# Kernel optimization log

Measured on AMD Instinct MI355X. Metric: run time of the kernel, lower is better.

Reference implementation:

```python
import jax, jax.numpy as jnp
import numpy as np

N_NODES = 100000
N_EDGES = 600000
VOCAB = 50000
EMBED_DIM = 128
HIDDEN_DIM = 128


def gcn_conv(h, W, b, src, dst, n_nodes):
    """PyG GCNConv: x' = D^{-1/2} (A+I) D^{-1/2} X W + b.
    src/dst already include self-loops."""
    hw = h @ W                                   # [N, out]
    deg = jnp.zeros((n_nodes,), hw.dtype).at[dst].add(1.0)   # in-degree incl. self-loop
    dinv = jax.lax.rsqrt(deg)                    # deg >= 1 thanks to self-loops
    norm = dinv[src] * dinv[dst]                 # [E+N]
    msgs = norm[:, None] * hw[src]               # gather [E+N, out]
    out = jnp.zeros_like(hw).at[dst].add(msgs)   # scatter-aggregate
    return out + b


def setup_inputs() -> dict:
    key = jax.random.key(0)
    ks = jax.random.split(key, 8)
    x = jax.random.randint(ks[0], (N_NODES,), 0, VOCAB, dtype=jnp.int64 if jax.config.jax_enable_x64 else jnp.int32)
    edge_index = jax.random.randint(ks[1], (2, N_EDGES), 0, N_NODES, dtype=jnp.int32)
    emb = jax.random.normal(ks[2], (VOCAB, EMBED_DIM), dtype=jnp.float32)
    # Glorot-style scale for GCN weights
    W1 = jax.random.normal(ks[3], (EMBED_DIM, HIDDEN_DIM), dtype=jnp.float32) * (1.0 / np.sqrt(EMBED_DIM))
    b1 = jnp.zeros((HIDDEN_DIM,), dtype=jnp.float32)
    W2 = jax.random.normal(ks[4], (HIDDEN_DIM, HIDDEN_DIM), dtype=jnp.float32) * (1.0 / np.sqrt(HIDDEN_DIM))
    b2 = jnp.zeros((HIDDEN_DIM,), dtype=jnp.float32)
    return {"x": x, "edge_index": edge_index, "emb": emb, "W1": W1, "b1": b1, "W2": W2, "b2": b2}


def reference(x, edge_index, emb, W1, b1, W2, b2):
    n = x.shape[0]
    loops = jnp.arange(n, dtype=edge_index.dtype)
    src = jnp.concatenate([edge_index[0], loops])  # add self-loops once
    dst = jnp.concatenate([edge_index[1], loops])
    h = emb[x]                                     # [N, embed_dim] embedding lookup
    h = jax.nn.relu(gcn_conv(h, W1, b1, src, dst, n))
    h = jax.nn.relu(gcn_conv(h, W2, b2, src, dst, n))
    return h
```

## Files before the change

### kernel.cpp

```cpp
#include <hip/hip_runtime.h>


#define NDIM 128
#define PAD_K 136
#define SCAN_IPT 4
#define SCAN_BLK 256
#define SCAN_IPB (SCAN_BLK * SCAN_IPT)

typedef __bf16 bf16x8 __attribute__((ext_vector_type(8)));
typedef __bf16 bf16x4 __attribute__((ext_vector_type(4)));
typedef float f32x4 __attribute__((ext_vector_type(4)));

__device__ __forceinline__ float bf2f(unsigned short u) {
    union { unsigned int i; float f; } c;
    c.i = (unsigned int)u << 16;
    return c.f;
}
__device__ __forceinline__ unsigned short f2bf(float f) {
    __bf16 b = (__bf16)f;
    return __builtin_bit_cast(unsigned short, b);
}

__global__ void degree_count(const int* __restrict__ dst, int* __restrict__ cnt, int E) {
    int e = blockIdx.x * blockDim.x + threadIdx.x;
    if (e < E) atomicAdd(&cnt[dst[e]], 1);
}

__global__ void scan_blocks(const int* __restrict__ in, int* __restrict__ out,
                            int* __restrict__ bsums, int n) {
    __shared__ int lds[SCAN_BLK];
    const int t = threadIdx.x;
    const int base = blockIdx.x * SCAN_IPB + t * SCAN_IPT;
    int v[SCAN_IPT];
    int s = 0;
#pragma unroll
    for (int k = 0; k < SCAN_IPT; ++k) { v[k] = (base + k < n) ? in[base + k] : 0; s += v[k]; }
    lds[t] = s;
    __syncthreads();
    for (int off = 1; off < SCAN_BLK; off <<= 1) {
        int x = (t >= off) ? lds[t - off] : 0;
        __syncthreads();
        lds[t] += x;
        __syncthreads();
    }
    if (t == SCAN_BLK - 1) bsums[blockIdx.x] = lds[t];
    int run = (t == 0) ? 0 : lds[t - 1];
#pragma unroll
    for (int k = 0; k < SCAN_IPT; ++k) {
        if (base + k < n) out[base + k] = run;
        run += v[k];
    }
}

__global__ void scan_partials(int* __restrict__ bsums, int nb) {
    __shared__ int lds[128];
    const int t = threadIdx.x;
    lds[t] = (t < nb) ? bsums[t] : 0;
    __syncthreads();
    for (int off = 1; off < 128; off <<= 1) {
        int x = (t >= off) ? lds[t - off] : 0;
        __syncthreads();
        lds[t] += x;
        __syncthreads();
    }
    if (t < nb) bsums[t] = (t == 0) ? 0 : lds[t - 1];
}

__global__ void add_offsets_dinv(int* __restrict__ rp, const int* __restrict__ bsums,
                                 const int* __restrict__ cnt, float* __restrict__ dinv,
                                 int n, int E) {
    int i = blockIdx.x * blockDim.x + threadIdx.x;
    if (i < n) {
        rp[i] += bsums[i / SCAN_IPB];
        dinv[i] = rsqrtf((float)cnt[i] + 1.0f);
    }
    if (i == 0) rp[n] = E;
}

__global__ void fill_edges(const int* __restrict__ src, const int* __restrict__ dst,
                           const int* __restrict__ rp, int* __restrict__ cur,
                           int* __restrict__ esrc, int E) {
    int e = blockIdx.x * blockDim.x + threadIdx.x;
    if (e >= E) return;
    int d = dst[e];
    int p = rp[d] + atomicAdd(&cur[d], 1);
    esrc[p] = src[e];
}

__global__ void wt_convert2(const float* __restrict__ W1, const float* __restrict__ W2,
                            unsigned short* __restrict__ WT1, unsigned short* __restrict__ WT2) {
    int c = blockIdx.x * blockDim.x + threadIdx.x;
    int cc = c & 16383;
    int j = cc >> 7, k = cc & 127;
    if (c < 16384) WT1[cc] = f2bf(W1[k * 128 + j]);
    else           WT2[cc] = f2bf(W2[k * 128 + j]);
}

template <int MODE, bool SCALE>
__global__ __launch_bounds__(256, 3)
void gemm_mfma(const void* __restrict__ Asrc, const unsigned short* __restrict__ WTb,
               const float* __restrict__ dinv, unsigned short* __restrict__ outb, int n) {
    __shared__ __bf16 sA[64 * PAD_K];
    __shared__ __bf16 sBT[128 * PAD_K];
    const int tid = threadIdx.x;
    const int rbase = blockIdx.x * 64;

    if (MODE == 0) {
        const float* A = (const float*)Asrc;
#pragma unroll
        for (int i = 0; i < 8; ++i) {
            int c = tid + i * 256;
            int r = c >> 5, c4 = c & 31;
            int gr = rbase + r;
            int srow = (gr < n) ? gr : (n - 1);
            float4 v = ((const float4*)A)[(size_t)srow * 32 + c4];
            bf16x4 w = { (__bf16)v.x, (__bf16)v.y, (__bf16)v.z, (__bf16)v.w };
            *(bf16x4*)&sA[r * PAD_K + c4 * 4] = w;
        }
    } else {
        const unsigned short* A = (const unsigned short*)Asrc;
#pragma unroll
        for (int i = 0; i < 4; ++i) {
            int c = tid + i * 256;
            int r = c >> 4, u = c & 15;
            int gr = rbase + r;
            int srow = (gr < n) ? gr : (n - 1);
            uint4 v = ((const uint4*)(A + (size_t)srow * 128))[u];
            *(uint4*)&sA[r * PAD_K + u * 8] = v;
        }
    }
    {
        const uint4* bsrc = (const uint4*)WTb;
#pragma unroll
        for (int i = 0; i < 8; ++i) {
            int c = tid + i * 256;
            int j = c >> 4, u = c & 15;
            *(uint4*)&sBT[j * PAD_K + u * 8] = bsrc[c];
        }
    }
    __syncthreads();

    const int wave = tid >> 6, lane = tid & 63;
    const int quad = lane >> 4, lrow = lane & 15;

    f32x4 acc[8];
#pragma unroll
    for (int nt = 0; nt < 8; ++nt) acc[nt] = (f32x4)0.0f;

#pragma unroll
    for (int ks = 0; ks < 4; ++ks) {
        const int kb = ks * 32 + quad * 8;
        bf16x8 a = *(const bf16x8*)&sA[(wave * 16 + lrow) * PAD_K + kb];
#pragma unroll
        for (int nt = 0; nt < 8; ++nt) {
            bf16x8 b = *(const bf16x8*)&sBT[(nt * 16 + lrow) * PAD_K + kb];
            acc[nt] = __builtin_amdgcn_mfma_f32_16x16x32_bf16(a, b, acc[nt], 0, 0, 0);
        }
    }

#pragma unroll
    for (int r = 0; r < 4; ++r) {
        int grow = rbase + wave * 16 + quad * 4 + r;
        if (grow < n) {
            float dsc = SCALE ? dinv[grow] : 1.0f;
            unsigned short* orow = outb + (size_t)grow * NDIM + lrow;
#pragma unroll
            for (int nt = 0; nt < 8; ++nt)
                orow[nt * 16] = f2bf(SCALE ? dsc * acc[nt][r] : acc[nt][r]);
        }
    }
}

__global__ void gather_scale(const unsigned short* __restrict__ tab, const int* __restrict__ x,
                             const float* __restrict__ dinv, unsigned short* __restrict__ vs,
                             int n) {
    int t = blockIdx.x * blockDim.x + threadIdx.x;
    int i = t >> 4, u = t & 15;
    if (i >= n) return;
    int row = x[i];
    float di = dinv[i];
    union { uint4 q; unsigned short s[8]; } a;
    a.q = ((const uint4*)(tab + (size_t)row * 128))[u];
#pragma unroll
    for (int k = 0; k < 8; ++k) a.s[k] = f2bf(di * bf2f(a.s[k]));
    ((uint4*)(vs + (size_t)i * 128))[u] = a.q;
}

template <bool OUT_BF16>
__global__ void aggregate_csr(const unsigned short* __restrict__ vs, const int* __restrict__ rp,
                              const int* __restrict__ esrc, const float* __restrict__ dinv,
                              const float* __restrict__ bias, void* __restrict__ out, int n) {
    int t = blockIdx.x * blockDim.x + threadIdx.x;
    int i = t >> 5, lane = t & 31;
    if (i >= n) return;
    const ushort4* vs4 = (const ushort4*)vs;
    ushort4 u = vs4[(size_t)i * 32 + lane];
    float4 acc = make_float4(bf2f(u.x), bf2f(u.y), bf2f(u.z), bf2f(u.w));
    int j = rp[i];
    const int end = rp[i + 1];
    for (; j + 4 <= end; j += 4) {
        int s0 = esrc[j], s1 = esrc[j + 1], s2 = esrc[j + 2], s3 = esrc[j + 3];
        ushort4 v0 = vs4[(size_t)s0 * 32 + lane];
        ushort4 v1 = vs4[(size_t)s1 * 32 + lane];
        ushort4 v2 = vs4[(size_t)s2 * 32 + lane];
        ushort4 v3 = vs4[(size_t)s3 * 32 + lane];
        acc.x += (bf2f(v0.x) + bf2f(v1.x)) + (bf2f(v2.x) + bf2f(v3.x));
        acc.y += (bf2f(v0.y) + bf2f(v1.y)) + (bf2f(v2.y) + bf2f(v3.y));
        acc.z += (bf2f(v0.z) + bf2f(v1.z)) + (bf2f(v2.z) + bf2f(v3.z));
        acc.w += (bf2f(v0.w) + bf2f(v1.w)) + (bf2f(v2.w) + bf2f(v3.w));
    }
    for (; j < end; ++j) {
        int s = esrc[j];
        ushort4 v = vs4[(size_t)s * 32 + lane];
        acc.x += bf2f(v.x);
        acc.y += bf2f(v.y);
        acc.z += bf2f(v.z);
        acc.w += bf2f(v.w);
    }
    float di = dinv[i];
    float4 b = ((const float4*)bias)[lane];
    acc.x = fmaxf(fmaf(di, acc.x, b.x), 0.0f);
    acc.y = fmaxf(fmaf(di, acc.y, b.y), 0.0f);
    acc.z = fmaxf(fmaf(di, acc.z, b.z), 0.0f);
    acc.w = fmaxf(fmaf(di, acc.w, b.w), 0.0f);
    if (OUT_BF16) {
        ushort4 o = make_ushort4(f2bf(acc.x), f2bf(acc.y), f2bf(acc.z), f2bf(acc.w));
        ((ushort4*)out)[(size_t)i * 32 + lane] = o;
    } else {
        ((float4*)out)[(size_t)i * 32 + lane] = acc;
    }
}

extern "C" void kernel_launch(void* const* d_in, const int* in_sizes, int n_in,
                              void* d_out, int out_size, void* d_ws, size_t ws_size,
                              hipStream_t stream) {
    const int* x = (const int*)d_in[0];
    const int* edge_index = (const int*)d_in[1];
    const float* emb = (const float*)d_in[2];
    const float* W1 = (const float*)d_in[3];
    const float* b1 = (const float*)d_in[4];
    const float* W2 = (const float*)d_in[5];
    const float* b2 = (const float*)d_in[6];
    float* out = (float*)d_out;

    const int N = in_sizes[0];
    const int E = in_sizes[1] / 2;
    const int V = in_sizes[2] / NDIM;
    const int* src = edge_index;
    const int* dst = edge_index + E;

    char* p = (char*)d_ws;
    auto alloc = [&](size_t bytes) {
        char* q = p;
        p += (bytes + 511) & ~(size_t)511;
        return q;
    };
    int* cnt = (int*)alloc((size_t)2 * N * sizeof(int));
    int* cur = cnt + N;
    int* rp = (int*)alloc((size_t)(N + 1) * sizeof(int));
    float* dinv = (float*)alloc((size_t)N * sizeof(float));
    int* bsums = (int*)alloc(128 * sizeof(int));
    int* esrc = (int*)alloc((size_t)E * sizeof(int));
    unsigned short* WT1 = (unsigned short*)alloc(16384 * sizeof(unsigned short));
    unsigned short* WT2 = (unsigned short*)alloc(16384 * sizeof(unsigned short));
    unsigned short* embW1 = (unsigned short*)alloc((size_t)V * NDIM * sizeof(unsigned short));
    unsigned short* vs1 = (unsigned short*)alloc((size_t)N * NDIM * sizeof(unsigned short));
    unsigned short* h1b = (unsigned short*)alloc((size_t)N * NDIM * sizeof(unsigned short));
    unsigned short* vs2 = (unsigned short*)alloc((size_t)N * NDIM * sizeof(unsigned short));
    (void)ws_size;

    const int NB = (N + SCAN_IPB - 1) / SCAN_IPB;

    hipMemsetAsync(cnt, 0, (size_t)2 * N * sizeof(int), stream);
    degree_count<<<(E + 255) / 256, 256, 0, stream>>>(dst, cnt, E);
    scan_blocks<<<NB, SCAN_BLK, 0, stream>>>(cnt, rp, bsums, N);
    scan_partials<<<1, 128, 0, stream>>>(bsums, NB);
    add_offsets_dinv<<<(N + 255) / 256, 256, 0, stream>>>(rp, bsums, cnt, dinv, N, E);
    fill_edges<<<(E + 255) / 256, 256, 0, stream>>>(src, dst, rp, cur, esrc, E);

    wt_convert2<<<128, 256, 0, stream>>>(W1, W2, WT1, WT2);

    const int agg_blocks = (int)(((size_t)N * 32 + 255) / 256);
    const int gs_blocks = (int)(((size_t)N * 16 + 255) / 256);

    gemm_mfma<0, false><<<(V + 63) / 64, 256, 0, stream>>>(emb, WT1, nullptr, embW1, V);
    gather_scale<<<gs_blocks, 256, 0, stream>>>(embW1, x, dinv, vs1, N);
    aggregate_csr<true><<<agg_blocks, 256, 0, stream>>>(vs1, rp, esrc, dinv, b1, h1b, N);
    gemm_mfma<1, true><<<(N + 63) / 64, 256, 0, stream>>>(h1b, WT2, dinv, vs2, N);
    aggregate_csr<false><<<agg_blocks, 256, 0, stream>>>(vs2, rp, esrc, dinv, b2, out, N);
}
```

Measured before the change: 258.4 us.

## Fuse embedding gather into layer-1 aggregation and streamline CSR build and GEMM loads

Removes the gather_scale kernel and its intermediate buffer. The first aggregation now reads the projected embedding table directly through a per-edge (vocab row, dinv) record written during CSR fill. The CSR fill uses atomicAdd on the row pointer itself, dropping the separate cursor array and the rp[n] write; row ranges become rp[i-1]..rp[i]. The GEMM drops the shared-memory A tile and loads A straight from global memory into registers, with launch bounds raised to 4 blocks per CU. Both aggregations now use 16 lanes per row with 16-byte loads. In exchange, fill_edges writes an extra 8 bytes per edge, and layer 1 gathers from the 50k-row table with per-edge scaling.

Measured after the change: 247.4 us. 4.2% less time.

```diff
diff --git a/kernel.cpp b/kernel.cpp
--- a/kernel.cpp
+++ b/kernel.cpp
@@ -8,7 +8,6 @@
 #define SCAN_IPB (SCAN_BLK * SCAN_IPT)
 
 typedef __bf16 bf16x8 __attribute__((ext_vector_type(8)));
-typedef __bf16 bf16x4 __attribute__((ext_vector_type(4)));
 typedef float f32x4 __attribute__((ext_vector_type(4)));
 
 __device__ __forceinline__ float bf2f(unsigned short u) {
@@ -19,6 +18,16 @@
 __device__ __forceinline__ unsigned short f2bf(float f) {
     __bf16 b = (__bf16)f;
     return __builtin_bit_cast(unsigned short, b);
+}
+__device__ __forceinline__ void unpack8(uint4 q, float* f) {
+    f[0] = bf2f((unsigned short)(q.x & 0xffff));
+    f[1] = bf2f((unsigned short)(q.x >> 16));
+    f[2] = bf2f((unsigned short)(q.y & 0xffff));
+    f[3] = bf2f((unsigned short)(q.y >> 16));
+    f[4] = bf2f((unsigned short)(q.z & 0xffff));
+    f[5] = bf2f((unsigned short)(q.z >> 16));
+    f[6] = bf2f((unsigned short)(q.w & 0xffff));
+    f[7] = bf2f((unsigned short)(q.w >> 16));
 }
 
 __global__ void degree_count(const int* __restrict__ dst, int* __restrict__ cnt, int E) {
@@ -67,24 +76,24 @@
 }
 
 __global__ void add_offsets_dinv(int* __restrict__ rp, const int* __restrict__ bsums,
-                                 const int* __restrict__ cnt, float* __restrict__ dinv,
-                                 int n, int E) {
+                                 const int* __restrict__ cnt, float* __restrict__ dinv, int n) {
     int i = blockIdx.x * blockDim.x + threadIdx.x;
     if (i < n) {
         rp[i] += bsums[i / SCAN_IPB];
         dinv[i] = rsqrtf((float)cnt[i] + 1.0f);
     }
-    if (i == 0) rp[n] = E;
 }
 
 __global__ void fill_edges(const int* __restrict__ src, const int* __restrict__ dst,
-                           const int* __restrict__ rp, int* __restrict__ cur,
-                           int* __restrict__ esrc, int E) {
+                           int* __restrict__ rp, const int* __restrict__ x,
+                           const float* __restrict__ dinv,
+                           int* __restrict__ esrc, int2* __restrict__ ew, int E) {
     int e = blockIdx.x * blockDim.x + threadIdx.x;
     if (e >= E) return;
-    int d = dst[e];
-    int p = rp[d] + atomicAdd(&cur[d], 1);
-    esrc[p] = src[e];
+    int d = dst[e], s = src[e];
+    int p = atomicAdd(&rp[d], 1);
+    esrc[p] = s;
+    ew[p] = make_int2(x[s], __float_as_int(dinv[s]));
 }
 
 __global__ void wt_convert2(const float* __restrict__ W1, const float* __restrict__ W2,
@@ -97,38 +106,13 @@
 }
 
 template <int MODE, bool SCALE>
-__global__ __launch_bounds__(256, 3)
+__global__ __launch_bounds__(256, 4)
 void gemm_mfma(const void* __restrict__ Asrc, const unsigned short* __restrict__ WTb,
                const float* __restrict__ dinv, unsigned short* __restrict__ outb, int n) {
-    __shared__ __bf16 sA[64 * PAD_K];
     __shared__ __bf16 sBT[128 * PAD_K];
     const int tid = threadIdx.x;
     const int rbase = blockIdx.x * 64;
 
-    if (MODE == 0) {
-        const float* A = (const float*)Asrc;
-#pragma unroll
-        for (int i = 0; i < 8; ++i) {
-            int c = tid + i * 256;
-            int r = c >> 5, c4 = c & 31;
-            int gr = rbase + r;
-            int srow = (gr < n) ? gr : (n - 1);
-            float4 v = ((const float4*)A)[(size_t)srow * 32 + c4];
-            bf16x4 w = { (__bf16)v.x, (__bf16)v.y, (__bf16)v.z, (__bf16)v.w };
-            *(bf16x4*)&sA[r * PAD_K + c4 * 4] = w;
-        }
-    } else {
-        const unsigned short* A = (const unsigned short*)Asrc;
-#pragma unroll
-        for (int i = 0; i < 4; ++i) {
-            int c = tid + i * 256;
-            int r = c >> 4, u = c & 15;
-            int gr = rbase + r;
-            int srow = (gr < n) ? gr : (n - 1);
-            uint4 v = ((const uint4*)(A + (size_t)srow * 128))[u];
-            *(uint4*)&sA[r * PAD_K + u * 8] = v;
-        }
-    }
     {
         const uint4* bsrc = (const uint4*)WTb;
 #pragma unroll
@@ -142,6 +126,8 @@
 
     const int wave = tid >> 6, lane = tid & 63;
     const int quad = lane >> 4, lrow = lane & 15;
+    int arow = rbase + wave * 16 + lrow;
+    if (arow >= n) arow = n - 1;
 
     f32x4 acc[8];
 #pragma unroll
@@ -150,7 +136,16 @@
 #pragma unroll
     for (int ks = 0; ks < 4; ++ks) {
         const int kb = ks * 32 + quad * 8;
-        bf16x8 a = *(const bf16x8*)&sA[(wave * 16 + lrow) * PAD_K + kb];
+        bf16x8 a;
+        if (MODE == 0) {
+            const float4* A4 = (const float4*)Asrc;
+            float4 v0 = A4[(size_t)arow * 32 + (kb >> 2)];
+            float4 v1 = A4[(size_t)arow * 32 + (kb >> 2) + 1];
+            a = (bf16x8){(__bf16)v0.x, (__bf16)v0.y, (__bf16)v0.z, (__bf16)v0.w,
+                         (__bf16)v1.x, (__bf16)v1.y, (__bf16)v1.z, (__bf16)v1.w};
+        } else {
+            a = *(const bf16x8*)((const unsigned short*)Asrc + (size_t)arow * 128 + kb);
+        }
 #pragma unroll
         for (int nt = 0; nt < 8; ++nt) {
             bf16x8 b = *(const bf16x8*)&sBT[(nt * 16 + lrow) * PAD_K + kb];
@@ -171,64 +166,113 @@
     }
 }
 
-__global__ void gather_scale(const unsigned short* __restrict__ tab, const int* __restrict__ x,
-                             const float* __restrict__ dinv, unsigned short* __restrict__ vs,
-                             int n) {
+__global__ void aggregate1(const unsigned short* __restrict__ tab, const int* __restrict__ x,
+                           const int* __restrict__ rp, const int2* __restrict__ ew,
+                           const float* __restrict__ dinv, const float* __restrict__ bias,
+                           unsigned short* __restrict__ outb, int n) {
     int t = blockIdx.x * blockDim.x + threadIdx.x;
     int i = t >> 4, u = t & 15;
     if (i >= n) return;
-    int row = x[i];
+    const uint4* tab4 = (const uint4*)tab;
     float di = dinv[i];
-    union { uint4 q; unsigned short s[8]; } a;
-    a.q = ((const uint4*)(tab + (size_t)row * 128))[u];
-#pragma unroll
-    for (int k = 0; k < 8; ++k) a.s[k] = f2bf(di * bf2f(a.s[k]));
-    ((uint4*)(vs + (size_t)i * 128))[u] = a.q;
-}
-
-template <bool OUT_BF16>
-__global__ void aggregate_csr(const unsigned short* __restrict__ vs, const int* __restrict__ rp,
-                              const int* __restrict__ esrc, const float* __restrict__ dinv,
-                              const float* __restrict__ bias, void* __restrict__ out, int n) {
+    float acc[8];
+    {
+        float f[8];
+        unpack8(tab4[(size_t)x[i] * 16 + u], f);
+#pragma unroll
+        for (int k = 0; k < 8; ++k) acc[k] = di * f[k];
+    }
+    int j = (i == 0) ? 0 : rp[i - 1];
+    const int end = rp[i];
+    for (; j + 4 <= end; j += 4) {
+        int2 e0 = ew[j], e1 = ew[j + 1], e2 = ew[j + 2], e3 = ew[j + 3];
+        uint4 q0 = tab4[(size_t)e0.x * 16 + u];
+        uint4 q1 = tab4[(size_t)e1.x * 16 + u];
+        uint4 q2 = tab4[(size_t)e2.x * 16 + u];
+        uint4 q3 = tab4[(size_t)e3.x * 16 + u];
+        float f0[8], f1[8], f2[8], f3[8];
+        unpack8(q0, f0); unpack8(q1, f1); unpack8(q2, f2); unpack8(q3, f3);
+        float n0 = __int_as_float(e0.y), n1 = __int_as_float(e1.y);
+        float n2 = __int_as_float(e2.y), n3 = __int_as_float(e3.y);
+#pragma unroll
+        for (int k = 0; k < 8; ++k) {
+            float s01 = fmaf(n0, f0[k], n1 * f1[k]);
+            float s23 = fmaf(n2, f2[k], n3 * f3[k]);
+            acc[k] += s01 + s23;
+        }
+    }
+    for (; j < end; ++j) {
+        int2 e = ew[j];
+        uint4 q = tab4[(size_t)e.x * 16 + u];
+        float f[8];
+        unpack8(q, f);
+        float nm = __int_as_float(e.y);
+#pragma unroll
+        for (int k = 0; k < 8; ++k) acc[k] = fmaf(nm, f[k], acc[k]);
+    }
+    const float4 b0 = ((const float4*)bias)[u * 2];
+    const float4 b1 = ((const float4*)bias)[u * 2 + 1];
+    float r[8];
+    r[0] = fmaxf(fmaf(di, acc[0], b0.x), 0.0f);
+    r[1] = fmaxf(fmaf(di, acc[1], b0.y), 0.0f);
+    r[2] = fmaxf(fmaf(di, acc[2], b0.z), 0.0f);
+    r[3] = fmaxf(fmaf(di, acc[3], b0.w), 0.0f);
+    r[4] = fmaxf(fmaf(di, acc[4], b1.x), 0.0f);
+    r[5] = fmaxf(fmaf(di, acc[5], b1.y), 0.0f);
+    r[6] = fmaxf(fmaf(di, acc[6], b1.z), 0.0f);
+    r[7] = fmaxf(fmaf(di, acc[7], b1.w), 0.0f);
+    uint4 o;
+    o.x = (unsigned)f2bf(r[0]) | ((unsigned)f2bf(r[1]) << 16);
+    o.y = (unsigned)f2bf(r[2]) | ((unsigned)f2bf(r[3]) << 16);
+    o.z = (unsigned)f2bf(r[4]) | ((unsigned)f2bf(r[5]) << 16);
+    o.w = (unsigned)f2bf(r[6]) | ((unsigned)f2bf(r[7]) << 16);
+    ((uint4*)outb)[(size_t)i * 16 + u] = o;
+}
+
+__global__ void aggregate2(const unsigned short* __restrict__ vs, const int* __restrict__ rp,
+                           const int* __restrict__ esrc, const float* __restrict__ dinv,
+                           const float* __restrict__ bias, float* __restrict__ out, int n) {
     int t = blockIdx.x * blockDim.x + threadIdx.x;
-    int i = t >> 5, lane = t & 31;
+    int i = t >> 4, u = t & 15;
     if (i >= n) return;
-    const ushort4* vs4 = (const ushort4*)vs;
-    ushort4 u = vs4[(size_t)i * 32 + lane];
-    float4 acc = make_float4(bf2f(u.x), bf2f(u.y), bf2f(u.z), bf2f(u.w));
-    int j = rp[i];
-    const int end = rp[i + 1];
+    const uint4* vs4 = (const uint4*)vs;
+    float acc[8];
+    unpack8(vs4[(size_t)i * 16 + u], acc);
+    int j = (i == 0) ? 0 : rp[i - 1];
+    const int end = rp[i];
     for (; j + 4 <= end; j += 4) {
         int s0 = esrc[j], s1 = esrc[j + 1], s2 = esrc[j + 2], s3 = esrc[j + 3];
-        ushort4 v0 = vs4[(size_t)s0 * 32 + lane];
-        ushort4 v1 = vs4[(size_t)s1 * 32 + lane];
-        ushort4 v2 = vs4[(size_t)s2 * 32 + lane];
-        ushort4 v3 = vs4[(size_t)s3 * 32 + lane];
-        acc.x += (bf2f(v0.x) + bf2f(v1.x)) + (bf2f(v2.x) + bf2f(v3.x));
-        acc.y += (bf2f(v0.y) + bf2f(v1.y)) + (bf2f(v2.y) + bf2f(v3.y));
-        acc.z += (bf2f(v0.z) + bf2f(v1.z)) + (bf2f(v2.z) + bf2f(v3.z));
-        acc.w += (bf2f(v0.w) + bf2f(v1.w)) + (bf2f(v2.w) + bf2f(v3.w));
+        uint4 q0 = vs4[(size_t)s0 * 16 + u];
+        uint4 q1 = vs4[(size_t)s1 * 16 + u];
+        uint4 q2 = vs4[(size_t)s2 * 16 + u];
+        uint4 q3 = vs4[(size_t)s3 * 16 + u];
+        float f0[8], f1[8], f2[8], f3[8];
+        unpack8(q0, f0); unpack8(q1, f1); unpack8(q2, f2); unpack8(q3, f3);
+#pragma unroll
+        for (int k = 0; k < 8; ++k) acc[k] += (f0[k] + f1[k]) + (f2[k] + f3[k]);
     }
     for (; j < end; ++j) {
         int s = esrc[j];
-        ushort4 v = vs4[(size_t)s * 32 + lane];
-        acc.x += bf2f(v.x);
-        acc.y += bf2f(v.y);
-        acc.z += bf2f(v.z);
-        acc.w += bf2f(v.w);
+        uint4 q = vs4[(size_t)s * 16 + u];
+        float f[8];
+        unpack8(q, f);
+#pragma unroll
+        for (int k = 0; k < 8; ++k) acc[k] += f[k];
     }
     float di = dinv[i];
-    float4 b = ((const float4*)bias)[lane];
-    acc.x = fmaxf(fmaf(di, acc.x, b.x), 0.0f);
-    acc.y = fmaxf(fmaf(di, acc.y, b.y), 0.0f);
-    acc.z = fmaxf(fmaf(di, acc.z, b.z), 0.0f);
-    acc.w = fmaxf(fmaf(di, acc.w, b.w), 0.0f);
-    if (OUT_BF16) {
-        ushort4 o = make_ushort4(f2bf(acc.x), f2bf(acc.y), f2bf(acc.z), f2bf(acc.w));
-        ((ushort4*)out)[(size_t)i * 32 + lane] = o;
-    } else {
-        ((float4*)out)[(size_t)i * 32 + lane] = acc;
-    }
+    const float4 b0 = ((const float4*)bias)[u * 2];
+    const float4 b1 = ((const float4*)bias)[u * 2 + 1];
+    float4 r0, r1;
+    r0.x = fmaxf(fmaf(di, acc[0], b0.x), 0.0f);
+    r0.y = fmaxf(fmaf(di, acc[1], b0.y), 0.0f);
+    r0.z = fmaxf(fmaf(di, acc[2], b0.z), 0.0f);
+    r0.w = fmaxf(fmaf(di, acc[3], b0.w), 0.0f);
+    r1.x = fmaxf(fmaf(di, acc[4], b1.x), 0.0f);
+    r1.y = fmaxf(fmaf(di, acc[5], b1.y), 0.0f);
+    r1.z = fmaxf(fmaf(di, acc[6], b1.z), 0.0f);
+    r1.w = fmaxf(fmaf(di, acc[7], b1.w), 0.0f);
+    ((float4*)out)[(size_t)i * 32 + u * 2] = r0;
+    ((float4*)out)[(size_t)i * 32 + u * 2 + 1] = r1;
 }
 
 extern "C" void kernel_launch(void* const* d_in, const int* in_sizes, int n_in,
@@ -255,37 +299,34 @@
         p += (bytes + 511) & ~(size_t)511;
         return q;
     };
-    int* cnt = (int*)alloc((size_t)2 * N * sizeof(int));
-    int* cur = cnt + N;
-    int* rp = (int*)alloc((size_t)(N + 1) * sizeof(int));
+    int* cnt = (int*)alloc((size_t)N * sizeof(int));
+    int* rp = (int*)alloc((size_t)N * sizeof(int));
     float* dinv = (float*)alloc((size_t)N * sizeof(float));
     int* bsums = (int*)alloc(128 * sizeof(int));
     int* esrc = (int*)alloc((size_t)E * sizeof(int));
+    int2* ew = (int2*)alloc((size_t)E * sizeof(int2));
     unsigned short* WT1 = (unsigned short*)alloc(16384 * sizeof(unsigned short));
     unsigned short* WT2 = (unsigned short*)alloc(16384 * sizeof(unsigned short));
     unsigned short* embW1 = (unsigned short*)alloc((size_t)V * NDIM * sizeof(unsigned short));
-    unsigned short* vs1 = (unsigned short*)alloc((size_t)N * NDIM * sizeof(unsigned short));
     unsigned short* h1b = (unsigned short*)alloc((size_t)N * NDIM * sizeof(unsigned short));
     unsigned short* vs2 = (unsigned short*)alloc((size_t)N * NDIM * sizeof(unsigned short));
     (void)ws_size;
 
     const int NB = (N + SCAN_IPB - 1) / SCAN_IPB;
 
-    hipMemsetAsync(cnt, 0, (size_t)2 * N * sizeof(int), stream);
+    hipMemsetAsync(cnt, 0, (size_t)N * sizeof(int), stream);
     degree_count<<<(E + 255) / 256, 256, 0, stream>>>(dst, cnt, E);
     scan_blocks<<<NB, SCAN_BLK, 0, stream>>>(cnt, rp, bsums, N);
     scan_partials<<<1, 128, 0, stream>>>(bsums, NB);
-    add_offsets_dinv<<<(N + 255) / 256, 256, 0, stream>>>(rp, bsums, cnt, dinv, N, E);
-    fill_edges<<<(E + 255) / 256, 256, 0, stream>>>(src, dst, rp, cur, esrc, E);
+    add_offsets_dinv<<<(N + 255) / 256, 256, 0, stream>>>(rp, bsums, cnt, dinv, N);
+    fill_edges<<<(E + 255) / 256, 256, 0, stream>>>(src, dst, rp, x, dinv, esrc, ew, E);
 
     wt_convert2<<<128, 256, 0, stream>>>(W1, W2, WT1, WT2);
 
-    const int agg_blocks = (int)(((size_t)N * 32 + 255) / 256);
-    const int gs_blocks = (int)(((size_t)N * 16 + 255) / 256);
+    const int agg_blocks = (int)(((size_t)N * 16 + 255) / 256);
 
     gemm_mfma<0, false><<<(V + 63) / 64, 256, 0, stream>>>(emb, WT1, nullptr, embW1, V);
-    gather_scale<<<gs_blocks, 256, 0, stream>>>(embW1, x, dinv, vs1, N);
-    aggregate_csr<true><<<agg_blocks, 256, 0, stream>>>(vs1, rp, esrc, dinv, b1, h1b, N);
+    aggregate1<<<agg_blocks, 256, 0, stream>>>(embW1, x, rp, ew, dinv, b1, h1b, N);
     gemm_mfma<1, true><<<(N + 63) / 64, 256, 0, stream>>>(h1b, WT2, dinv, vs2, N);
-    aggregate_csr<false><<<agg_blocks, 256, 0, stream>>>(vs2, rp, esrc, dinv, b2, out, N);
-}
+    aggregate2<<<agg_blocks, 256, 0, stream>>>(vs2, rp, esrc, dinv, b2, out, N);
+}
```
